# Optimization experiments

Measured on AMD Instinct MI355X. Metric: run time of the kernel, lower is better.

The kernel has to match this reference:

```python
import jax, jax.numpy as jnp
import numpy as np

N_IMG = 8
IMG_H = IMG_W = 1024
STRIDES = (4, 8, 16, 32, 64)
FEAT = tuple(IMG_H // s for s in STRIDES)
RATIOS = (0.5, 1.0, 2.0)
A = len(RATIOS)
PRE_NMS = 1000
POST_NMS = 1000
NMS_THRESH = 0.7
SCORE_THRESH = 0.0
MIN_SIZE = 1e-3
BBOX_CLIP = float(np.log(1000.0 / 16.0))  # torchvision bbox_xform_clip
NPL = tuple(f * f * A for f in FEAT)      # anchors per level


def _make_anchors():
    levels = []
    for stride, f in zip(STRIDES, FEAT):
        size = stride * 8.0
        base = []
        for r in RATIOS:
            w = size * np.sqrt(1.0 / r)
            h = size * np.sqrt(r)
            base.append([-w / 2, -h / 2, w / 2, h / 2])
        base = np.asarray(base, np.float32)              # [A,4]
        coords = np.arange(f, dtype=np.float32) * stride
        sy, sx = np.meshgrid(coords, coords, indexing="ij")
        shifts = np.stack([sx, sy, sx, sy], -1).reshape(-1, 1, 4)  # y-major, matches [H,W,A] flatten
        levels.append((shifts + base[None]).reshape(-1, 4))
    return np.concatenate(levels, 0).astype(np.float32)


def setup_inputs() -> dict:
    key = jax.random.key(0)
    ks = jax.random.split(key, 10)
    inp = {}
    for i, f in enumerate(FEAT):
        inp[f"obj_l{i}"] = jax.random.normal(ks[i], (N_IMG, A, f, f), jnp.float32)
        inp[f"delta_l{i}"] = jax.random.normal(ks[5 + i], (N_IMG, A * 4, f, f), jnp.float32) * 0.2
    inp["anchors"] = jnp.asarray(_make_anchors())
    return inp


def _flatten_level(obj, delta):
    # permute_and_flatten: [N,A,H,W] -> [N,H*W*A] ; [N,A*4,H,W] -> [N,H*W*A,4]
    n, a, h, w = obj.shape
    o = jnp.transpose(obj, (0, 2, 3, 1)).reshape(n, -1)
    d = jnp.transpose(delta.reshape(n, a, 4, h, w), (0, 3, 4, 1, 2)).reshape(n, -1, 4)
    return o, d


def _decode(deltas, anchors):
    # BoxCoder(weights=(1,1,1,1)).decode
    w = anchors[:, 2] - anchors[:, 0]
    h = anchors[:, 3] - anchors[:, 1]
    cx = anchors[:, 0] + 0.5 * w
    cy = anchors[:, 1] + 0.5 * h
    dx, dy = deltas[..., 0], deltas[..., 1]
    dw = jnp.minimum(deltas[..., 2], BBOX_CLIP)
    dh = jnp.minimum(deltas[..., 3], BBOX_CLIP)
    pcx = dx * w + cx
    pcy = dy * h + cy
    pw = jnp.exp(dw) * w
    ph = jnp.exp(dh) * h
    return jnp.stack([pcx - 0.5 * pw, pcy - 0.5 * ph, pcx + 0.5 * pw, pcy + 0.5 * ph], -1)


def _nms_image(boxes, scores, lvl):
    # clip_boxes_to_image
    x1 = jnp.clip(boxes[:, 0], 0.0, IMG_W)
    y1 = jnp.clip(boxes[:, 1], 0.0, IMG_H)
    x2 = jnp.clip(boxes[:, 2], 0.0, IMG_W)
    y2 = jnp.clip(boxes[:, 3], 0.0, IMG_H)
    boxes = jnp.stack([x1, y1, x2, y2], -1)
    # remove_small_boxes + score_thresh, as a mask (fixed shapes)
    valid = (x2 - x1 >= MIN_SIZE) & (y2 - y1 >= MIN_SIZE) & (scores >= SCORE_THRESH)
    s = jnp.where(valid, scores, -1.0)
    order = jnp.argsort(-s)
    boxes, s, valid, lvl = boxes[order], s[order], valid[order], lvl[order]
    # batched_nms: offset boxes per level so cross-level IoU is 0
    ob = boxes + (lvl.astype(boxes.dtype) * (max(IMG_H, IMG_W) + 1.0))[:, None]
    ob = jax.lax.stop_gradient(ob)  # keep decisions are non-differentiable
    area = (ob[:, 2] - ob[:, 0]) * (ob[:, 3] - ob[:, 1])
    lt = jnp.maximum(ob[:, None, :2], ob[None, :, :2])
    rb = jnp.minimum(ob[:, None, 2:], ob[None, :, 2:])
    wh = jnp.maximum(rb - lt, 0.0)
    inter = wh[..., 0] * wh[..., 1]
    iou = inter / (area[:, None] + area[None, :] - inter + 1e-9)  # [K,K]
    k = boxes.shape[0]
    jidx = jnp.arange(k)

    def body(i, keep):
        sup = keep[i] & (iou[i] > NMS_THRESH) & (jidx > i)
        return keep & ~sup

    keep = jax.lax.fori_loop(0, k, body, valid)
    # compact kept boxes (score-sorted) into fixed [POST_NMS] output, zero-padded
    rank = jnp.cumsum(keep) - 1
    tgt = jnp.where(keep & (rank < POST_NMS), rank, POST_NMS)
    out_b = jnp.zeros((POST_NMS + 1, 4), boxes.dtype).at[tgt].set(boxes)[:POST_NMS]
    out_s = jnp.zeros((POST_NMS + 1,), s.dtype).at[tgt].set(jnp.where(keep, s, 0.0))[:POST_NMS]
    return out_b, out_s


def _forward(objs, deltas, anchors):
    flat = [_flatten_level(o, d) for o, d in zip(objs, deltas)]
    obj = jnp.concatenate([f[0] for f in flat], 1)       # [N, K_total]
    dl = jnp.concatenate([f[1] for f in flat], 1)        # [N, K_total, 4]
    proposals = _decode(dl, anchors)                     # [N, K_total, 4]
    lvl_full = jnp.concatenate([jnp.full((n,), i, jnp.int32) for i, n in enumerate(NPL)])
    # per-level top-k on objectness logits
    idxs, off = [], 0
    for n in NPL:
        kk = min(PRE_NMS, n)
        _, ti = jax.lax.top_k(obj[:, off:off + n], kk)
        idxs.append(ti + off)
        off += n
    top_idx = jnp.concatenate(idxs, 1)                   # [N, K_sel]
    scores = jax.nn.sigmoid(jnp.take_along_axis(obj, top_idx, 1))
    prop = jnp.take_along_axis(proposals, top_idx[..., None], 1)
    lvl = lvl_full[top_idx]
    boxes_out, _ = jax.lax.map(lambda t: _nms_image(*t), (prop, scores, lvl))
    return boxes_out                                     # [N, POST_NMS, 4]


def reference(obj_l0, obj_l1, obj_l2, obj_l3, obj_l4, delta_l0, delta_l1, delta_l2, delta_l3, delta_l4, anchors):
    return _forward([obj_l0, obj_l1, obj_l2, obj_l3, obj_l4],
                    [delta_l0, delta_l1, delta_l2, delta_l3, delta_l4], anchors)
```

## Files before the change

### kernel.cpp

```cpp
#include <hip/hip_runtime.h>
#include <cstdint>

#define K_SEL 4768
#define CAND_CAP 16384
#define NBIN 4096
#define BUFCAP 512
#define TPAD 9216

struct P5 { const float* p[5]; };

__device__ __forceinline__ unsigned fsortkey(float f) {
  unsigned b = __float_as_uint(f);
  return (b & 0x80000000u) ? ~b : (b | 0x80000000u);
}

__global__ __launch_bounds__(256) void k_hist(P5 obj, unsigned* phist) {
  int p = blockIdx.y; int img = p / 5, lvl = p % 5;
  int f = 256 >> lvl; int n = 3 * f * f;
  __shared__ unsigned lh[NBIN];
  for (int b = threadIdx.x; b < NBIN; b += 256) lh[b] = 0;
  __syncthreads();
  const float4* src4 = (const float4*)(obj.p[lvl] + (size_t)img * n);
  int n4 = n >> 2;
  int chunk = (n4 + gridDim.x - 1) / gridDim.x;
  int e0 = blockIdx.x * chunk, e1 = min(n4, e0 + chunk);
  for (int e = e0 + threadIdx.x; e < e1; e += 256) {
    float4 v = src4[e];
    atomicAdd(&lh[fsortkey(v.x) >> 20], 1u);
    atomicAdd(&lh[fsortkey(v.y) >> 20], 1u);
    atomicAdd(&lh[fsortkey(v.z) >> 20], 1u);
    atomicAdd(&lh[fsortkey(v.w) >> 20], 1u);
  }
  __syncthreads();
  unsigned* dst = phist + ((size_t)(p * 8 + blockIdx.x)) * NBIN;
  for (int b = threadIdx.x; b < NBIN; b += 256) dst[b] = lh[b];
}

__global__ __launch_bounds__(256) void k_thresh(const unsigned* phist, int* Bthr, unsigned* cnt) {
  int p = blockIdx.x; int lvl = p % 5;
  unsigned kk = (lvl == 4) ? 768u : 1000u;
  __shared__ unsigned hsum[NBIN];
  __shared__ unsigned csum[256];
  int c = threadIdx.x;
  unsigned tot[16];
#pragma unroll
  for (int k = 0; k < 16; ++k) tot[k] = 0;
  for (int g = 0; g < 8; ++g) {
    const unsigned* hp = phist + ((size_t)(p * 8 + g)) * NBIN + c * 16;
#pragma unroll
    for (int k = 0; k < 16; ++k) tot[k] += hp[k];
  }
  unsigned s = 0;
#pragma unroll
  for (int k = 0; k < 16; ++k) { hsum[c * 16 + k] = tot[k]; s += tot[k]; }
  csum[c] = s;
  __syncthreads();
  if (c == 0) {
    unsigned acc = 0; int B = 0;
    for (int cc = 255; cc >= 0; --cc) {
      if (acc + csum[cc] >= kk) {
        for (int b = 15; b >= 0; --b) {
          acc += hsum[cc * 16 + b];
          if (acc >= kk) { B = cc * 16 + b; break; }
        }
        break;
      }
      acc += csum[cc];
    }
    Bthr[p] = B;
    cnt[p] = 0;
  }
}

__global__ __launch_bounds__(256) void k_gather(P5 obj, const int* Bthr, unsigned* cnt,
                                                unsigned long long* ck) {
  int p = blockIdx.y; int img = p / 5, lvl = p % 5;
  int f = 256 >> lvl; int hw = f * f; int n = 3 * hw;
  int B = Bthr[p];
  int shift = 2 * (8 - lvl);
  const float4* src4 = (const float4*)(obj.p[lvl] + (size_t)img * n);
  int n4 = n >> 2;
  unsigned long long* dst = ck + (size_t)p * CAND_CAP;
  int tid = threadIdx.x;
  int lane = tid & 63, wv = tid >> 6;
  __shared__ unsigned long long buf[4][BUFCAP];
  __shared__ unsigned wTot[4];
  __shared__ unsigned blkBase;
  unsigned wc = 0;
  for (int e = blockIdx.x * 256 + tid; e < n4; e += gridDim.x * 256) {
    float4 v = src4[e];
    float vv[4] = {v.x, v.y, v.z, v.w};
#pragma unroll
    for (int j = 0; j < 4; ++j) {
      unsigned sv = fsortkey(vv[j]);
      bool pass = (int)(sv >> 20) >= B;
      unsigned long long m = __ballot(pass);
      if (m) {
        if (pass) {
          unsigned pos = wc + (unsigned)__popcll(m & ((1ULL << lane) - 1ULL));
          int ee = e * 4 + j;
          int a = ee >> shift;
          int r = ee & (hw - 1);
          unsigned kidx = (unsigned)(r * 3 + a);
          unsigned long long key = ((unsigned long long)sv << 32) | (0xFFFFFFFFu - kidx);
          if (pos < BUFCAP) buf[wv][pos] = key;
          else {
            unsigned gp = atomicAdd(&cnt[p], 1u);
            if (gp < CAND_CAP) dst[gp] = key;
          }
        }
        wc += (unsigned)__popcll(m);
      }
    }
  }
  if (lane == 0) wTot[wv] = min(wc, (unsigned)BUFCAP);
  __syncthreads();
  if (tid == 0) {
    unsigned tot = wTot[0] + wTot[1] + wTot[2] + wTot[3];
    blkBase = tot ? atomicAdd(&cnt[p], tot) : 0u;
  }
  __syncthreads();
  unsigned myOff = blkBase;
  for (int x = 0; x < wv; ++x) myOff += wTot[x];
  unsigned wn = wTot[wv];
  for (unsigned j = lane; j < wn; j += 64) {
    unsigned gp = myOff + j;
    if (gp < CAND_CAP) dst[gp] = buf[wv][j];
  }
}

__global__ __launch_bounds__(256) void k_select(const unsigned* cnt, const unsigned long long* ck,
                                                unsigned* selSV, unsigned* selIdx) {
  int p = blockIdx.y; int img = p / 5, lvl = p % 5;
  int Cc = min((int)cnt[p], CAND_CAP);
  if (blockIdx.x * 256 >= Cc) return;
  int kk = (lvl == 4) ? 768 : 1000;
  int soff = lvl * 1000;
  const unsigned long long* keys = ck + (size_t)p * CAND_CAP;
  __shared__ unsigned long long sk[4096];
  int stage = min(Cc, 4096);
  for (int j = threadIdx.x; j < stage; j += 256) sk[j] = keys[j];
  __syncthreads();
  int c = blockIdx.x * 256 + threadIdx.x;
  if (c >= Cc) return;
  unsigned long long kc = keys[c];
  int rank = 0;
#pragma unroll 8
  for (int j = 0; j < stage; ++j) rank += (sk[j] > kc) ? 1 : 0;
  for (int j = stage; j < Cc; ++j) rank += (keys[j] > kc) ? 1 : 0;
  if (rank < kk) {
    int slot = img * K_SEL + soff + rank;
    selSV[slot]  = (unsigned)(kc >> 32);
    selIdx[slot] = 0xFFFFFFFFu - (unsigned)kc;
  }
}

__global__ __launch_bounds__(256) void k_decode(P5 del, const float* anchors,
                                                const unsigned* selSV, const unsigned* selIdx,
                                                float* boxP, unsigned long long* keyP) {
  int i = blockIdx.x * 256 + threadIdx.x;
  if (i >= K_SEL) return;
  int img = blockIdx.y;
  int lvl = (i < 4000) ? (i / 1000) : 4;
  int f = 256 >> lvl, hw = f * f;
  const int aoffA[5] = {0, 196608, 245760, 258048, 261120};
  int slot = img * K_SEL + i;
  unsigned k = selIdx[slot];
  unsigned sv = selSV[slot];
  int a = (int)(k % 3u); int r = (int)(k / 3u);
  int y = r >> (8 - lvl); int x = r & (f - 1);
  const float* dp = del.p[lvl] + (size_t)(img * 12 + a * 4) * hw + (size_t)y * f + x;
  float d0 = dp[0], d1 = dp[hw], d2 = dp[2 * hw], d3 = dp[3 * hw];
  const float* ar = anchors + (size_t)(aoffA[lvl] + (int)k) * 4;
  float a0 = ar[0], a1 = ar[1], a2 = ar[2], a3 = ar[3];
  float w = __fsub_rn(a2, a0), h = __fsub_rn(a3, a1);
  float cx = __fadd_rn(a0, __fmul_rn(0.5f, w));
  float cy = __fadd_rn(a1, __fmul_rn(0.5f, h));
  const float CLIP = 4.135166556742356f;
  float dw = fminf(d2, CLIP), dh = fminf(d3, CLIP);
  float pcx = __fadd_rn(__fmul_rn(d0, w), cx);
  float pcy = __fadd_rn(__fmul_rn(d1, h), cy);
  float pw = __fmul_rn(expf(dw), w);
  float ph = __fmul_rn(expf(dh), h);
  float x1 = __fsub_rn(pcx, __fmul_rn(0.5f, pw));
  float y1 = __fsub_rn(pcy, __fmul_rn(0.5f, ph));
  float x2 = __fadd_rn(pcx, __fmul_rn(0.5f, pw));
  float y2 = __fadd_rn(pcy, __fmul_rn(0.5f, ph));
  float x1c = fminf(fmaxf(x1, 0.0f), 1024.0f);
  float y1c = fminf(fmaxf(y1, 0.0f), 1024.0f);
  float x2c = fminf(fmaxf(x2, 0.0f), 1024.0f);
  float y2c = fminf(fmaxf(y2, 0.0f), 1024.0f);
  bool valid = (__fsub_rn(x2c, x1c) >= 1e-3f) && (__fsub_rn(y2c, y1c) >= 1e-3f);
  float* bp = boxP + (size_t)slot * 4;
  bp[0] = x1c; bp[1] = y1c; bp[2] = x2c; bp[3] = y2c;
  unsigned low = 0xFFFFFFFFu - (unsigned)i;
  keyP[slot] = valid ? (((unsigned long long)sv << 32) | low) : (unsigned long long)low;
}

__device__ __forceinline__ bool iou_gt(float rx1, float ry1, float rx2, float ry2, float rar,
                                       float cx1, float cy1, float cx2, float cy2, float car) {
  float ltx = fmaxf(rx1, cx1), lty = fmaxf(ry1, cy1);
  float rbx = fminf(rx2, cx2), rby = fminf(ry2, cy2);
  float wx = fmaxf(__fsub_rn(rbx, ltx), 0.0f);
  float wy = fmaxf(__fsub_rn(rby, lty), 0.0f);
  float inter = __fmul_rn(wx, wy);
  float denom = __fadd_rn(__fsub_rn(__fadd_rn(rar, car), inter), 1e-9f);
  return __fdiv_rn(inter, denom) > 0.7f;
}

__global__ __launch_bounds__(64) void k_lvlmask(const float* boxP, unsigned long long* T) {
  int img = blockIdx.y;
  int q = blockIdx.x;
  int lvl, q2;
  if (q < 544) { lvl = q / 136; q2 = q - lvl * 136; }
  else         { lvl = 4;       q2 = q - 544; }
  int kk = (lvl == 4) ? 768 : 1000;
  int nch = (kk + 63) >> 6;
  int rb = 0;
  while (q2 >= nch - rb) { q2 -= nch - rb; ++rb; }
  int cb = rb + q2;
  int t = threadIdx.x;
  float off = __fmul_rn((float)lvl, 1025.0f);
  const float4* b4 = (const float4*)boxP + (size_t)img * K_SEL + lvl * 1000;
  __shared__ float rx1s[64], ry1s[64], rx2s[64], ry2s[64], rars[64];
  int j = rb * 64 + t;
  if (j < kk) {
    float4 bb = b4[j];
    float ox1 = __fadd_rn(bb.x, off), oy1 = __fadd_rn(bb.y, off);
    float ox2 = __fadd_rn(bb.z, off), oy2 = __fadd_rn(bb.w, off);
    rx1s[t] = ox1; ry1s[t] = oy1; rx2s[t] = ox2; ry2s[t] = oy2;
    rars[t] = __fmul_rn(__fsub_rn(ox2, ox1), __fsub_rn(oy2, oy1));
  }
  __syncthreads();
  int i = cb * 64 + t;
  if (i >= kk) return;
  float4 bb = b4[i];
  float cx1 = __fadd_rn(bb.x, off), cy1 = __fadd_rn(bb.y, off);
  float cx2 = __fadd_rn(bb.z, off), cy2 = __fadd_rn(bb.w, off);
  float car = __fmul_rn(__fsub_rn(cx2, cx1), __fsub_rn(cy2, cy1));
  int jmaxR = min(64, kk - rb * 64);
  int jend = (rb == cb) ? min(t, jmaxR) : jmaxR;
  unsigned long long bits = 0;
  for (int jj = 0; jj < jend; ++jj) {
    if (iou_gt(rx1s[jj], ry1s[jj], rx2s[jj], ry2s[jj], rars[jj], cx1, cy1, cx2, cy2, car))
      bits |= (1ULL << jj);
  }
  const int Pt[16] = {0, 1, 4, 7, 12, 17, 24, 31, 40, 49, 60, 71, 84, 97, 112, 127};
  int sc = (cb + 1) | 1;
  T[(size_t)(img * 5 + lvl) * TPAD + 64 * Pt[cb] + t * sc + rb] = bits;
}

__global__ __launch_bounds__(256) void k_lvlnms(const unsigned long long* keyP,
                                                const unsigned long long* Tg_,
                                                unsigned long long* keepw) {
  int p = blockIdx.x; int img = p / 5, lvl = p % 5;
  int kk = (lvl == 4) ? 768 : 1000;
  int tw = (lvl == 4) ? 5376 : TPAD;
  int tid = threadIdx.x;
  int lane = tid & 63, wv = tid >> 6;
  __shared__ __align__(16) unsigned long long Ts[TPAD];
  __shared__ unsigned long long Us[16], Ks[16];
  const unsigned long long* Tg = Tg_ + (size_t)p * TPAD;
  for (int x = tid; x < (tw >> 1); x += 256)
    ((ulonglong2*)Ts)[x] = ((const ulonglong2*)Tg)[x];
  const unsigned long long* kp = keyP + (size_t)img * K_SEL + lvl * 1000;
#pragma unroll
  for (int jb = 0; jb < 4; ++jb) {
    int i = jb * 256 + tid;
    bool valid = (i < kk) && ((kp[min(i, kk - 1)] >> 32) != 0ULL);
    unsigned long long m = __ballot(valid);
    if (lane == 0) { int wi = jb * 4 + wv; Us[wi] = m; Ks[wi] = 0ULL; }
  }
  __syncthreads();
  const int Pt[16] = {0, 1, 4, 7, 12, 17, 24, 31, 40, 49, 60, 71, 84, 97, 112, 127};
  while (true) {
    unsigned long long us[16], ks[16], ku[16], uAny = 0;
#pragma unroll
    for (int w = 0; w < 16; ++w) {
      us[w] = Us[w]; ks[w] = Ks[w]; ku[w] = us[w] | ks[w]; uAny |= us[w];
    }
    __syncthreads();
    if (uAny == 0ULL) break;
#pragma unroll
    for (int jb = 0; jb < 4; ++jb) {
      int i = jb * 256 + tid;
      bool inU = (i < kk) && ((us[i >> 6] >> (i & 63)) & 1ULL);
      bool kept = false, dead = false;
      if (inU) {
        int ci = i >> 6, il = i & 63;
        int base = 64 * Pt[ci] + il * ((ci + 1) | 1);
        unsigned long long a = 0, b = 0;
        for (int w = 0; w <= ci; ++w) {
          unsigned long long tv = Ts[base + w];
          a |= tv & ku[w]; b |= tv & ks[w];
        }
        kept = (a == 0ULL);
        dead = !kept && (b != 0ULL);
      }
      unsigned long long mk = __ballot(kept), md = __ballot(dead);
      if (lane == 0) {
        int wi = jb * 4 + wv;
        Ks[wi] |= mk;
        Us[wi] &= ~(mk | md);
      }
    }
    __syncthreads();
  }
  if (tid < 16) keepw[(size_t)p * 16 + tid] = Ks[tid];
}

__global__ __launch_bounds__(256) void k_merge(const unsigned long long* keyP, const float* boxP,
                                               const unsigned long long* keepw, float* out) {
  int p = blockIdx.x; int img = p / 5, lvl = p % 5;
  int tid = threadIdx.x;
  __shared__ unsigned long long lkey[5000];
  __shared__ int lpos[5000];
  __shared__ int wp[5][17];
  __shared__ unsigned long long kwS[80];
  for (int x = tid; x < 80; x += 256) {
    int l = x >> 4, w = x & 15;
    kwS[x] = (l == 4 && w >= 12) ? 0ULL : keepw[(size_t)img * 80 + x];
  }
  __syncthreads();
  if (tid < 5) {
    int acc = 0;
    for (int w = 0; w < 16; ++w) { wp[tid][w] = acc; acc += (int)__popcll(kwS[tid * 16 + w]); }
    wp[tid][16] = acc;
  }
  __syncthreads();
  const unsigned long long* kp = keyP + (size_t)img * K_SEL;
  for (int i = tid; i < K_SEL; i += 256) {
    int l = (i < 4000) ? i / 1000 : 4;
    int li = i - l * 1000;
    unsigned long long wmask = kwS[l * 16 + (li >> 6)];
    if ((wmask >> (li & 63)) & 1ULL) {
      int j = wp[l][li >> 6] + (int)__popcll(wmask & ((1ULL << (li & 63)) - 1ULL));
      lkey[l * 1000 + j] = kp[i];
      lpos[l * 1000 + j] = i;
    }
  }
  __syncthreads();
  const float4* b4 = (const float4*)boxP + (size_t)img * K_SEL;
  float4* out4 = (float4*)out + (size_t)img * 1000;
  int kn = wp[lvl][16];
  for (int j = tid; j < kn; j += 256) {
    unsigned long long key = lkey[lvl * 1000 + j];
    int grank = j;
#pragma unroll
    for (int l2 = 0; l2 < 5; ++l2) {
      if (l2 == lvl) continue;
      int lo = 0, hi = wp[l2][16];
      const unsigned long long* a = &lkey[l2 * 1000];
      while (lo < hi) { int mid = (lo + hi) >> 1; if (a[mid] > key) lo = mid + 1; else hi = mid; }
      grank += lo;
    }
    if (grank < 1000) out4[grank] = b4[lpos[lvl * 1000 + j]];
  }
  if (lvl == 0) {
    int KT = wp[0][16] + wp[1][16] + wp[2][16] + wp[3][16] + wp[4][16];
    for (int s = min(KT, 1000) + tid; s < 1000; s += 256)
      out4[s] = make_float4(0.f, 0.f, 0.f, 0.f);
  }
}

extern "C" void kernel_launch(void* const* d_in, const int* in_sizes, int n_in,
                              void* d_out, int out_size, void* d_ws, size_t ws_size,
                              hipStream_t stream) {
  (void)in_sizes; (void)n_in;
  P5 obj, del;
  for (int i = 0; i < 5; ++i) {
    obj.p[i] = (const float*)d_in[2 * i];
    del.p[i] = (const float*)d_in[2 * i + 1];
  }
  const float* anchors = (const float*)d_in[10];
  float* out = (float*)d_out;
  char* ws = (char*)d_ws;

  unsigned* cnt               = (unsigned*)(ws + 0);
  int* Bthr                   = (int*)(ws + 192);
  unsigned long long* candK   = (unsigned long long*)(ws + 512);
  unsigned* selSV             = (unsigned*)(ws + 5243392);
  unsigned* selIdx            = (unsigned*)(ws + 5395968);
  float* boxP                 = (float*)(ws + 5548544);
  unsigned long long* keyP    = (unsigned long long*)(ws + 6158848);
  unsigned long long* keepw   = (unsigned long long*)(ws + 6464000);
  unsigned long long* T       = (unsigned long long*)(ws + 6469120);
  unsigned* phist             = (unsigned*)(ws + 6469120);
  const size_t NEED = 11712000ULL;
  if (ws_size < NEED) { hipMemsetAsync(d_out, 0, (size_t)out_size * 4, stream); return; }

  k_hist    <<<dim3(8, 40), 256, 0, stream>>>(obj, phist);
  k_thresh  <<<40, 256, 0, stream>>>(phist, Bthr, cnt);
  k_gather  <<<dim3(32, 40), 256, 0, stream>>>(obj, Bthr, cnt, candK);
  k_select  <<<dim3(64, 40), 256, 0, stream>>>(cnt, candK, selSV, selIdx);
  k_decode  <<<dim3(19, 8), 256, 0, stream>>>(del, anchors, selSV, selIdx, boxP, keyP);
  k_lvlmask <<<dim3(622, 8), 64, 0, stream>>>(boxP, T);
  k_lvlnms  <<<40, 256, 0, stream>>>(keyP, T, keepw);
  k_merge   <<<40, 256, 0, stream>>>(keyP, boxP, keepw, out);
}
```

Before: 251.1 us.

## Replace block-wide iterative NMS fixed-point with single-wavefront chunked ballot sweep

```diff
diff --git a/kernel.cpp b/kernel.cpp
--- a/kernel.cpp
+++ b/kernel.cpp
@@ -257,56 +257,55 @@
   int kk = (lvl == 4) ? 768 : 1000;
   int tw = (lvl == 4) ? 5376 : TPAD;
   int tid = threadIdx.x;
-  int lane = tid & 63, wv = tid >> 6;
   __shared__ __align__(16) unsigned long long Ts[TPAD];
-  __shared__ unsigned long long Us[16], Ks[16];
   const unsigned long long* Tg = Tg_ + (size_t)p * TPAD;
+  const unsigned long long* kp = keyP + (size_t)img * K_SEL + lvl * 1000;
+  unsigned vmask = 0;
+  if (tid < 64) {
+#pragma unroll
+    for (int c = 0; c < 16; ++c) {
+      int i = c * 64 + tid;
+      bool v = (i < kk) && ((kp[min(i, kk - 1)] >> 32) != 0ULL);
+      vmask |= v ? (1u << c) : 0u;
+    }
+  }
   for (int x = tid; x < (tw >> 1); x += 256)
     ((ulonglong2*)Ts)[x] = ((const ulonglong2*)Tg)[x];
-  const unsigned long long* kp = keyP + (size_t)img * K_SEL + lvl * 1000;
-#pragma unroll
-  for (int jb = 0; jb < 4; ++jb) {
-    int i = jb * 256 + tid;
-    bool valid = (i < kk) && ((kp[min(i, kk - 1)] >> 32) != 0ULL);
-    unsigned long long m = __ballot(valid);
-    if (lane == 0) { int wi = jb * 4 + wv; Us[wi] = m; Ks[wi] = 0ULL; }
-  }
-  __syncthreads();
+  __syncthreads();
+  if (tid >= 64) return;
+  int t = tid;
   const int Pt[16] = {0, 1, 4, 7, 12, 17, 24, 31, 40, 49, 60, 71, 84, 97, 112, 127};
-  while (true) {
-    unsigned long long us[16], ks[16], ku[16], uAny = 0;
-#pragma unroll
-    for (int w = 0; w < 16; ++w) {
-      us[w] = Us[w]; ks[w] = Ks[w]; ku[w] = us[w] | ks[w]; uAny |= us[w];
-    }
-    __syncthreads();
-    if (uAny == 0ULL) break;
-#pragma unroll
-    for (int jb = 0; jb < 4; ++jb) {
-      int i = jb * 256 + tid;
-      bool inU = (i < kk) && ((us[i >> 6] >> (i & 63)) & 1ULL);
-      bool kept = false, dead = false;
-      if (inU) {
-        int ci = i >> 6, il = i & 63;
-        int base = 64 * Pt[ci] + il * ((ci + 1) | 1);
-        unsigned long long a = 0, b = 0;
-        for (int w = 0; w <= ci; ++w) {
-          unsigned long long tv = Ts[base + w];
-          a |= tv & ku[w]; b |= tv & ks[w];
-        }
-        kept = (a == 0ULL);
-        dead = !kept && (b != 0ULL);
+  unsigned long long kw[16];
+#pragma unroll
+  for (int w = 0; w < 16; ++w) kw[w] = 0ULL;
+#pragma unroll
+  for (int c = 0; c < 16; ++c) {
+    if (c * 64 < kk) {
+      int base = 64 * Pt[c] + t * ((c + 1) | 1);
+      unsigned long long tv[16];
+#pragma unroll
+      for (int w = 0; w < 16; ++w) tv[w] = Ts[base + w];
+      unsigned long long a = 0;
+#pragma unroll
+      for (int w = 0; w < 16; ++w) a |= tv[w] & kw[w];
+      unsigned long long colT = tv[c];
+      bool alive = ((vmask >> c) & 1u) && (a == 0ULL);
+      unsigned long long keepm = 0ULL;
+      unsigned long long actm = __ballot(alive);
+      while (actm) {
+        bool cank = alive && ((colT & actm) == 0ULL);
+        unsigned long long newk = __ballot(cank);
+        keepm |= newk;
+        alive = alive && !cank && ((colT & newk) == 0ULL);
+        actm = __ballot(alive);
       }
-      unsigned long long mk = __ballot(kept), md = __ballot(dead);
-      if (lane == 0) {
-        int wi = jb * 4 + wv;
-        Ks[wi] |= mk;
-        Us[wi] &= ~(mk | md);
-      }
-    }
-    __syncthreads();
-  }
-  if (tid < 16) keepw[(size_t)p * 16 + tid] = Ks[tid];
+      kw[c] = keepm;
+    }
+  }
+  if (t == 0) {
+#pragma unroll
+    for (int c = 0; c < 16; ++c) keepw[(size_t)p * 16 + c] = kw[c];
+  }
 }
 
 __global__ __launch_bounds__(256) void k_merge(const unsigned long long* keyP, const float* boxP,
@@ -318,8 +317,7 @@
   __shared__ int wp[5][17];
   __shared__ unsigned long long kwS[80];
   for (int x = tid; x < 80; x += 256) {
-    int l = x >> 4, w = x & 15;
-    kwS[x] = (l == 4 && w >= 12) ? 0ULL : keepw[(size_t)img * 80 + x];
+    kwS[x] = keepw[(size_t)img * 80 + x];
   }
   __syncthreads();
   if (tid < 5) {
```

Measured after the change: 221.3 us. 1.14x faster.
